# Performance work log

Hardware: AMD Instinct MI355X
Metric: run time of the kernel (lower is better)

Reference implementation:

```python
import jax, jax.numpy as jnp
import numpy as np

B = 32
M = 3
MAG_DIM = 20
STD = 0.28
INV = float(1.0 / (np.sqrt(2.0) * STD))
NORM = float(1.0 / (np.sqrt(2.0 * np.pi) * STD))


def _lrelu(x):
    return jax.nn.leaky_relu(x, 0.01)


def _conv(x, w, b):
    y = jax.lax.conv_general_dilated(x, w, (2, 2), 'VALID',
                                     dimension_numbers=('NCHW', 'OIHW', 'NCHW'))
    return _lrelu(y + b[None, :, None, None])


def _combos(x):
    # x: [N, c, d] -> [N, c, c, 2d], pairs[n, i, j] = concat(x[n, i], x[n, j])
    # (matches torch getCombinations: tensorB = expand-over-i, tensorA = expand-over-j)
    N, c, d = x.shape
    left = jnp.broadcast_to(x[:, :, None, :], (N, c, c, d))
    right = jnp.broadcast_to(x[:, None, :, :], (N, c, c, d))
    return jnp.concatenate([left, right], axis=-1)


def _forward(batch, conv_w1, conv_b1, conv_w2, conv_b2, conv_w3, conv_b3, conv_w4, conv_b4,
             post_w, post_b, g_w1, g_b1, g_w2, g_b2, g_w3, g_b3, g_w4, g_b4,
             h_w1, h_b1, h_w2, h_b2, h_w3, h_b3, f_w1, f_b1, f_w2, f_b2, ff_w, ff_b):
    bsz = batch.shape[0]
    x = batch.reshape(bsz * 16, 1, 80, 80)
    # magnitude encoding (computed under no_grad in the original)
    mag = jnp.linspace(-1.0, 1.0, MAG_DIM).astype(batch.dtype)  # [20]
    t = jnp.tanh(x * (2.0 / 255.0) - 1.0)                        # [N,1,80,80]
    enc = NORM * jnp.exp(-(((t + mag[None, :, None, None]) * INV) ** 2))  # [N,20,80,80]
    enc = jax.lax.stop_gradient(enc)
    y = _conv(enc, conv_w1, conv_b1)   # [N,32,39,39]
    y = _conv(y, conv_w2, conv_b2)     # [N,32,19,19]
    y = _conv(y, conv_w3, conv_b3)     # [N,32,9,9]
    y = _conv(y, conv_w4, conv_b4)     # [N,32,4,4]
    obj = y.reshape(bsz * 16, 512) @ post_w + post_b             # [N,247]
    panel = obj.reshape(bsz, 16, 247)
    given, options = panel[:, :8], panel[:, 8:]
    giv = jnp.broadcast_to(given[:, None], (bsz, 8, 8, 247))
    ctx = jnp.concatenate([giv, options[:, :, None, :]], axis=2)  # [B,8,9,247]
    tags = jnp.broadcast_to(jnp.eye(9, dtype=batch.dtype), (bsz * 8, 9, 9))
    objects = jnp.concatenate([ctx.reshape(bsz * 8, 9, 247), tags], axis=-1)  # [B*8,9,256]

    z = _combos(objects).reshape(-1, 512)  # [B*8*81, 512]
    z = _lrelu(z @ g_w1 + g_b1)
    z = _lrelu(z @ g_w2 + g_b2)
    z = _lrelu(z @ g_w3 + g_b3)
    z = _lrelu(z @ g_w4 + g_b4)
    sum_j = z.reshape(bsz * 8, 9, 9, 256).sum(axis=2)  # [B*8,9,256]
    for i in range(h_w1.shape[0]):
        p = _combos(sum_j).reshape(-1, 512)
        z = _lrelu(p @ h_w1[i] + h_b1[i])
        z = _lrelu(z @ h_w2[i] + h_b2[i])
        z = _lrelu(z @ h_w3[i] + h_b3[i])
        sum_j = z.reshape(bsz * 8, 9, 9, 256).sum(axis=2)
    h_sum = sum_j.sum(axis=1)                          # [B*8,256]
    z = _lrelu(h_sum @ f_w1 + f_b1)
    z = _lrelu(z @ f_w2 + f_b2)
    result = z @ ff_w + ff_b                           # [B*8,1]
    answer = result.reshape(bsz, 8)
    loss = jnp.mean(h_sum ** 2) + jnp.mean(result ** 2)
    return answer, loss


def setup_inputs():
    key = jax.random.key(0)
    ks = iter(jax.random.split(key, 40))

    def U(shape, fan_in):
        s = 1.0 / np.sqrt(fan_in)
        return jax.random.uniform(next(ks), shape, jnp.float32, -s, s)

    inp = {
        'batch': jax.random.uniform(next(ks), (B, 16, 80, 80), jnp.float32, 0.0, 255.0),
        'conv_w1': U((32, MAG_DIM, 3, 3), MAG_DIM * 9), 'conv_b1': U((32,), MAG_DIM * 9),
        'conv_w2': U((32, 32, 3, 3), 288), 'conv_b2': U((32,), 288),
        'conv_w3': U((32, 32, 3, 3), 288), 'conv_b3': U((32,), 288),
        'conv_w4': U((32, 32, 3, 3), 288), 'conv_b4': U((32,), 288),
        'post_w': U((512, 247), 512), 'post_b': U((247,), 512),
        'g_w1': U((512, 512), 512), 'g_b1': U((512,), 512),
        'g_w2': U((512, 512), 512), 'g_b2': U((512,), 512),
        'g_w3': U((512, 512), 512), 'g_b3': U((512,), 512),
        'g_w4': U((512, 256), 512), 'g_b4': U((256,), 512),
        'h_w1': U((M, 512, 256), 512), 'h_b1': U((M, 256), 512),
        'h_w2': U((M, 256, 256), 256), 'h_b2': U((M, 256), 256),
        'h_w3': U((M, 256, 256), 256), 'h_b3': U((M, 256), 256),
        'f_w1': U((256, 256), 256), 'f_b1': U((256,), 256),
        'f_w2': U((256, 256), 256), 'f_b2': U((256,), 256),
        'ff_w': U((256, 1), 256), 'ff_b': U((1,), 256),
    }
    return inp


def reference(batch, conv_w1, conv_b1, conv_w2, conv_b2, conv_w3, conv_b3, conv_w4, conv_b4,
              post_w, post_b, g_w1, g_b1, g_w2, g_b2, g_w3, g_b3, g_w4, g_b4,
              h_w1, h_b1, h_w2, h_b2, h_w3, h_b3, f_w1, f_b1, f_w2, f_b2, ff_w, ff_b):
    return _forward(batch, conv_w1, conv_b1, conv_w2, conv_b2, conv_w3, conv_b3, conv_w4, conv_b4,
                    post_w, post_b, g_w1, g_b1, g_w2, g_b2, g_w3, g_b3, g_w4, g_b4,
                    h_w1, h_b1, h_w2, h_b2, h_w3, h_b3, f_w1, f_b1, f_w2, f_b2, ff_w, ff_b)
```

## Files before the change

### kernel.cpp

```cpp
#include <hip/hip_runtime.h>
#include <hip/hip_bf16.h>
#include <math.h>

static __device__ __forceinline__ float lrelu(float v){ return v > 0.0f ? v : 0.01f*v; }

static __device__ __forceinline__ unsigned short f2bf(float f){
  unsigned int u = __float_as_uint(f);
  unsigned int r = (u + 0x7fffu + ((u >> 16) & 1u)) >> 16;
  return (unsigned short)r;
}
static __device__ __forceinline__ float bf2f(unsigned short u){
  return __uint_as_float(((unsigned int)u) << 16);
}
static __device__ __forceinline__ unsigned int pack_bf2(float lo, float hi){
  __hip_bfloat162 bb = __float22bfloat162_rn(make_float2(lo, hi));
  return *reinterpret_cast<unsigned int*>(&bb);
}
static __device__ __forceinline__ void gload16(const void* g, void* l){
  __builtin_amdgcn_global_load_lds(
    (const __attribute__((address_space(1))) void*)(const void*)g,
    (__attribute__((address_space(3))) void*)l, 16, 0, 0);
}

#define ENC_NORM 1.4247939f
#define GC_C     6.3775511f
#define GC_2CD   1.3426423f
#define GC_CD2   0.070665395f
#define GC_S1    0.86820227f

typedef __attribute__((ext_vector_type(4))) float f32x4;
typedef __attribute__((ext_vector_type(8))) short bf16x8;

__global__ __launch_bounds__(256) void k_prep(
    const float* __restrict__ g_w1, const float* __restrict__ g_w2,
    const float* __restrict__ g_w3, const float* __restrict__ g_w4,
    const float* __restrict__ h_w1, const float* __restrict__ h_w2,
    const float* __restrict__ h_w3, const float* __restrict__ post_w,
    const float* __restrict__ conv_w2, const float* __restrict__ conv_w3,
    const float* __restrict__ conv_w4, const float* __restrict__ conv_w1,
    const float* __restrict__ f_w1, const float* __restrict__ f_w2,
    unsigned short* __restrict__ WT)
{
  int e = blockIdx.x*256 + threadIdx.x;
  float v;
  if (e < 262144) {
    int nn = e >> 8, kk = e & 255;
    v = (nn < 512) ? g_w1[kk*512 + nn] : g_w1[(256+kk)*512 + (nn-512)];
  } else if (e < 524288) {
    int r = e - 262144; int nn = r >> 9, kk = r & 511;
    v = g_w2[kk*512 + nn];
  } else if (e < 786432) {
    int r = e - 524288; int nn = r >> 9, kk = r & 511;
    v = g_w3[kk*512 + nn];
  } else if (e < 917504) {
    int r = e - 786432; int nn = r >> 9, kk = r & 511;
    v = g_w4[kk*256 + nn];
  } else if (e < 1310720) {
    int r = e - 917504; int i = r >> 17; int q = r & 131071;
    int nn = q >> 8, kk = q & 255;
    v = (nn < 256) ? h_w1[i*131072 + kk*256 + nn]
                   : h_w1[i*131072 + (256+kk)*256 + (nn-256)];
  } else if (e < 1507328) {
    int r = e - 1310720; int i = r >> 16; int q = r & 65535;
    int nn = q >> 8, kk = q & 255;
    v = h_w2[i*65536 + kk*256 + nn];
  } else if (e < 1703936) {
    int r = e - 1507328; int i = r >> 16; int q = r & 65535;
    int nn = q >> 8, kk = q & 255;
    v = h_w3[i*65536 + kk*256 + nn];
  } else if (e < 1835008) {
    int r = e - 1703936; int np = r >> 9, kp = r & 511;
    int px = kp >> 5, c = kp & 31;
    v = (np < 247) ? post_w[(c*16+px)*247 + np] : 0.f;
  } else if (e < 1862656) {
    int r = e - 1835008; int which = r / 9216; int q = r % 9216;
    int tap = q >> 10, o = (q >> 5) & 31, c = q & 31;
    const float* w = which==0 ? conv_w2 : (which==1 ? conv_w3 : conv_w4);
    v = w[(o*32+c)*9 + tap];
  } else if (e < 1871872) {
    int r = e - 1862656; int tap = r >> 10, o = (r >> 5) & 31, c = r & 31;
    v = (c < 20) ? conv_w1[(o*20+c)*9 + tap] : 0.f;
  } else if (e < 1937408) {
    int r = e - 1871872; int nn = r >> 8, kk = r & 255;
    v = f_w1[kk*256 + nn];
  } else {
    int r = e - 1937408; int nn = r >> 8, kk = r & 255;
    v = f_w2[kk*256 + nn];
  }
  WT[e] = f2bf(v);
}

__global__ __launch_bounds__(256, 1) void k_conv1m(
    const float* __restrict__ batch, const unsigned short* __restrict__ wc1,
    const float* __restrict__ bias, unsigned short* __restrict__ y)
{
  __shared__ unsigned short ench[7][80][40];
  int n = blockIdx.x;
  int s0 = blockIdx.y ? 7 : 0;
  int s1 = blockIdx.y ? 13 : 7;
  int tid = threadIdx.x;
  int lane = tid & 63, wid = tid >> 6;
  int lr = lane & 15, kg = lane >> 4;

  bf16x8 bf0[9], bf1[9];
  #pragma unroll
  for (int tap = 0; tap < 9; ++tap) {
    bf0[tap] = *(const bf16x8*)&wc1[tap*1024 + lr*32 + kg*8];
    bf1[tap] = *(const bf16x8*)&wc1[tap*1024 + (16+lr)*32 + kg*8];
  }
  float b0 = bias[lr], b1 = bias[16 + lr];
  const float S2 = GC_S1 * GC_S1;

  for (int s = s0; s < s1; ++s) {
    int orow0 = s * 3;
    int irow0 = orow0 * 2;
    const float* img = batch + (size_t)n*6400 + irow0*80;
    for (int p = tid; p < 7*80; p += 256) {
      int row = p / 80, hx = p % 80;
      int col = (hx < 40) ? 2*hx : 2*(hx-40)+1;
      if (col > 78) continue;
      float x = img[row*80 + col];
      float E = __expf(x * (4.0f/255.0f) - 2.0f);
      float t = 1.0f - 2.0f*__builtin_amdgcn_rcpf(E + 1.0f);
      float z = t - 1.0f;
      float e = ENC_NORM * __expf(-GC_C*z*z);
      float rg = __expf(-GC_2CD*z - GC_CD2);
      unsigned int pk[16];
      #pragma unroll
      for (int cp = 0; cp < 10; ++cp) {
        float e1 = e * rg;
        pk[cp] = pack_bf2(e, e1);
        e  = e1 * rg * GC_S1;
        rg = rg * S2;
      }
      #pragma unroll
      for (int cp = 10; cp < 16; ++cp) pk[cp] = 0u;
      unsigned short* dst = &ench[row][hx][0];
      *(uint4*)(dst)      = *(uint4*)&pk[0];
      *(uint4*)(dst + 8)  = *(uint4*)&pk[4];
      *(uint4*)(dst + 16) = *(uint4*)&pk[8];
      *(uint4*)(dst + 24) = *(uint4*)&pk[12];
    }
    __syncthreads();

    const int totpx = 117;
    for (int t = wid; t < 8; t += 4) {
      int pa = t*16 + lr;
      int pc = (pa < totpx) ? pa : (totpx - 1);
      int oh = pc / 39, ow = pc % 39;
      f32x4 acc0 = {0.f,0.f,0.f,0.f}, acc1 = {0.f,0.f,0.f,0.f};
      #pragma unroll
      for (int kh = 0; kh < 3; ++kh) {
        int r = oh*2 + kh;
        #pragma unroll
        for (int kw = 0; kw < 3; ++kw) {
          int hidx = (kw == 1) ? (40 + ow) : (ow + (kw >> 1));
          bf16x8 a = *(const bf16x8*)&ench[r][hidx][kg*8];
          int tap = kh*3 + kw;
          acc0 = __builtin_amdgcn_mfma_f32_16x16x32_bf16(a, bf0[tap], acc0, 0, 0, 0);
          acc1 = __builtin_amdgcn_mfma_f32_16x16x32_bf16(a, bf1[tap], acc1, 0, 0, 0);
        }
      }
      #pragma unroll
      for (int rr = 0; rr < 4; ++rr) {
        int ps = t*16 + kg*4 + rr;
        if (ps < totpx) {
          int soh = orow0 + ps / 39, sow = ps % 39;
          unsigned short* op = y + (((size_t)n*39 + soh)*39 + sow)*32;
          op[lr]      = f2bf(lrelu(acc0[rr] + b0));
          op[16 + lr] = f2bf(lrelu(acc1[rr] + b1));
        }
      }
    }
    __syncthreads();
  }
}

template<int H, int W, int OH, int OW, int ROWS, int SLABS>
__global__ __launch_bounds__(256, 1) void k_cmfma(
    const unsigned short* __restrict__ in, const unsigned short* __restrict__ wc,
    const float* __restrict__ bias, unsigned short* __restrict__ out)
{
  constexpr int IR = 2*ROWS + 1;
  constexpr int EV = (W + 1) / 2;
  __shared__ unsigned short xs[IR][W][40];
  int n = blockIdx.x;
  int tid = threadIdx.x;
  int lane = tid & 63, wid = tid >> 6;
  int lr = lane & 15, kg = lane >> 4;

  bf16x8 bf0[9], bf1[9];
  #pragma unroll
  for (int tap = 0; tap < 9; ++tap) {
    bf0[tap] = *(const bf16x8*)&wc[(tap*32 + lr)*32      + kg*8];
    bf1[tap] = *(const bf16x8*)&wc[(tap*32 + 16 + lr)*32 + kg*8];
  }
  float b0 = bias[lr], b1 = bias[16 + lr];

  for (int s = 0; s < SLABS; ++s) {
    int orow0 = (blockIdx.y * SLABS + s) * ROWS;
    if (orow0 >= OH) break;
    int nrows = min(ROWS, OH - orow0);
    int irow0 = orow0 * 2;
    int ir = min(2*nrows + 1, H - irow0);

    const unsigned short* ip = in + ((size_t)n*H + irow0)*W*32;
    int npx = ir * W;
    for (int p = tid; p < npx; p += 256) {
      const uint4* src = (const uint4*)(ip + (size_t)p*32);
      uint4 v0 = src[0], v1 = src[1], v2 = src[2], v3 = src[3];
      int r = p / W, col = p % W;
      int hx = (col & 1) ? EV + (col >> 1) : (col >> 1);
      unsigned short* dst = &xs[r][hx][0];
      *(uint4*)(dst)      = v0;
      *(uint4*)(dst + 8)  = v1;
      *(uint4*)(dst + 16) = v2;
      *(uint4*)(dst + 24) = v3;
    }
    __syncthreads();

    int totpx = nrows * OW;
    int ntiles = (totpx + 15) >> 4;
    for (int t = wid; t < ntiles; t += 4) {
      int pa = t*16 + lr;
      int pc = (pa < totpx) ? pa : 0;
      int oh = pc / OW, ow = pc % OW;
      f32x4 acc0 = {0.f,0.f,0.f,0.f}, acc1 = {0.f,0.f,0.f,0.f};
      #pragma unroll
      for (int kh = 0; kh < 3; ++kh)
        #pragma unroll
        for (int kw = 0; kw < 3; ++kw) {
          int hidx = (kw == 1) ? (EV + ow) : (ow + (kw >> 1));
          bf16x8 a = *(const bf16x8*)&xs[oh*2 + kh][hidx][kg*8];
          acc0 = __builtin_amdgcn_mfma_f32_16x16x32_bf16(a, bf0[kh*3+kw], acc0, 0, 0, 0);
          acc1 = __builtin_amdgcn_mfma_f32_16x16x32_bf16(a, bf1[kh*3+kw], acc1, 0, 0, 0);
        }
      #pragma unroll
      for (int rr = 0; rr < 4; ++rr) {
        int ps = t*16 + kg*4 + rr;
        if (ps < totpx) {
          int soh = orow0 + ps / OW, sow = ps % OW;
          unsigned short* op = out + (((size_t)n*OH + soh)*OW + sow)*32;
          op[lr]      = f2bf(lrelu(acc0[rr] + b0));
          op[16 + lr] = f2bf(lrelu(acc1[rr] + b1));
        }
      }
    }
    __syncthreads();
  }
}

template<int OUT_BF16, int ACT>
__global__ __launch_bounds__(256) void k_mgemm(
    const unsigned short* __restrict__ A, const unsigned short* __restrict__ Wt,
    const float* __restrict__ bias, void* __restrict__ Cv,
    int M, int N, int K)
{
  __shared__ unsigned short As[128*64];
  __shared__ unsigned short Bs[128*64];
  int bm = blockIdx.x * 128;
  int bn = blockIdx.y * 128;
  int tid = threadIdx.x;
  int wid = tid >> 6, lane = tid & 63;
  int wr = (wid >> 1) * 64, wc = (wid & 1) * 64;
  int lr = lane & 15, kg = lane >> 4;

  int srow = lane >> 3;
  int ssw  = ((lane & 7) * 16) ^ (srow << 4);
  int rsw  = (lr & 7) << 4;

  f32x4 acc[4][4];
  #pragma unroll
  for (int i = 0; i < 4; ++i)
    #pragma unroll
    for (int j = 0; j < 4; ++j)
      acc[i][j] = (f32x4){0.f,0.f,0.f,0.f};

  for (int k0 = 0; k0 < K; k0 += 64) {
    #pragma unroll
    for (int i = 0; i < 4; ++i) {
      int rowc = wid*32 + i*8;
      int row  = rowc + srow;
      gload16((const char*)&A[(size_t)(bm + row)*K + k0] + ssw, &As[rowc*64]);
      gload16((const char*)&Wt[(size_t)(bn + row)*K + k0] + ssw, &Bs[rowc*64]);
    }
    __syncthreads();
    #pragma unroll
    for (int ks = 0; ks < 2; ++ks) {
      int roff = ((ks*64 + kg*16) ^ rsw) >> 1;
      bf16x8 a[4], b[4];
      #pragma unroll
      for (int i = 0; i < 4; ++i) {
        a[i] = *(const bf16x8*)&As[(wr + i*16 + lr)*64 + roff];
        b[i] = *(const bf16x8*)&Bs[(wc + i*16 + lr)*64 + roff];
      }
      #pragma unroll
      for (int i = 0; i < 4; ++i)
        #pragma unroll
        for (int j = 0; j < 4; ++j)
          acc[i][j] = __builtin_amdgcn_mfma_f32_16x16x32_bf16(a[i], b[j], acc[i][j], 0, 0, 0);
    }
    __syncthreads();
  }
  int r0 = (lane >> 4) * 4;
  #pragma unroll
  for (int i = 0; i < 4; ++i) {
    #pragma unroll
    for (int j = 0; j < 4; ++j) {
      int col = bn + wc + j*16 + lr;
      float bv = bias ? bias[col] : 0.f;
      #pragma unroll
      for (int rr = 0; rr < 4; ++rr) {
        int row = bm + wr + i*16 + r0 + rr;
        float v = acc[i][j][rr] + bv;
        if (ACT) v = lrelu(v);
        if (OUT_BF16) ((unsigned short*)Cv)[(size_t)row*N + col] = f2bf(v);
        else          ((float*)Cv)[(size_t)row*N + col] = v;
      }
    }
  }
}

__global__ __launch_bounds__(256) void k_pgemm(
    const unsigned short* __restrict__ UV, const unsigned short* __restrict__ Wt,
    const float* __restrict__ abias, const float* __restrict__ obias,
    unsigned short* __restrict__ C, int M, int N, int K)
{
  __shared__ unsigned short As[128*64];
  __shared__ unsigned short Bs[128*64];
  __shared__ float absm[512];
  int bm = blockIdx.x * 128;
  int bn = blockIdx.y * 128;
  int tid = threadIdx.x;
  int wid = tid >> 6, lane = tid & 63;
  int wr = (wid >> 1) * 64, wc = (wid & 1) * 64;
  int lr = lane & 15, kg = lane >> 4;
  int ld = 2*K;

  int srow = lane >> 3;
  int ssw  = ((lane & 7) * 16) ^ (srow << 4);
  int rsw  = (lr & 7) << 4;

  for (int idx = tid; idx < K; idx += 256) absm[idx] = abias[idx];

  int urow[4], vrow[4], arow[4], asw[4];
  #pragma unroll
  for (int i = 0; i < 4; ++i) {
    int ch = tid + (i << 8);
    int r = ch >> 3;
    int m = bm + r;
    int n = m / 81; int rem = m - n*81;
    int ii = rem / 9; int jj = rem - ii*9;
    urow[i] = n*9 + ii; vrow[i] = n*9 + jj;
    arow[i] = r;
    asw[i] = (((ch & 7) * 16) ^ ((r & 7) << 4)) >> 1;
  }
  __syncthreads();

  f32x4 acc[4][4];
  #pragma unroll
  for (int i = 0; i < 4; ++i)
    #pragma unroll
    for (int j = 0; j < 4; ++j)
      acc[i][j] = (f32x4){0.f,0.f,0.f,0.f};

  for (int k0 = 0; k0 < K; k0 += 64) {
    #pragma unroll
    for (int i = 0; i < 4; ++i) {
      int rowc = wid*32 + i*8;
      int row  = rowc + srow;
      gload16((const char*)&Wt[(size_t)(bn + row)*K + k0] + ssw, &Bs[rowc*64]);
    }
    #pragma unroll
    for (int i = 0; i < 4; ++i) {
      int ch = tid + (i << 8);
      int kc = (ch & 7) * 8;
      uint4 u4 = *(const uint4*)&UV[(size_t)urow[i]*ld + k0 + kc];
      uint4 v4 = *(const uint4*)&UV[(size_t)vrow[i]*ld + K + k0 + kc];
      const unsigned short* us = (const unsigned short*)&u4;
      const unsigned short* vs = (const unsigned short*)&v4;
      unsigned int pk[4];
      #pragma unroll
      for (int e2 = 0; e2 < 4; ++e2) {
        float a0 = bf2f(us[2*e2])   + bf2f(vs[2*e2])   + absm[k0 + kc + 2*e2];
        float a1 = bf2f(us[2*e2+1]) + bf2f(vs[2*e2+1]) + absm[k0 + kc + 2*e2+1];
        pk[e2] = pack_bf2(lrelu(a0), lrelu(a1));
      }
      *(uint4*)&As[arow[i]*64 + asw[i]] = *(uint4*)pk;
    }
    __syncthreads();
    #pragma unroll
    for (int ks = 0; ks < 2; ++ks) {
      int roff = ((ks*64 + kg*16) ^ rsw) >> 1;
      bf16x8 a[4], b[4];
      #pragma unroll
      for (int i = 0; i < 4; ++i) {
        a[i] = *(const bf16x8*)&As[(wr + i*16 + lr)*64 + roff];
        b[i] = *(const bf16x8*)&Bs[(wc + i*16 + lr)*64 + roff];
      }
      #pragma unroll
      for (int i = 0; i < 4; ++i)
        #pragma unroll
        for (int j = 0; j < 4; ++j)
          acc[i][j] = __builtin_amdgcn_mfma_f32_16x16x32_bf16(a[i], b[j], acc[i][j], 0, 0, 0);
    }
    __syncthreads();
  }
  int r0 = (lane >> 4) * 4;
  #pragma unroll
  for (int i = 0; i < 4; ++i) {
    #pragma unroll
    for (int j = 0; j < 4; ++j) {
      int col = bn + wc + j*16 + lr;
      float bv = obias[col];
      #pragma unroll
      for (int rr = 0; rr < 4; ++rr) {
        int row = bm + wr + i*16 + r0 + rr;
        C[(size_t)row*N + col] = f2bf(lrelu(acc[i][j][rr] + bv));
      }
    }
  }
}

__global__ void k_objects(const float* __restrict__ panel, const float* __restrict__ post_b,
                          unsigned short* __restrict__ obj)
{
  int idx = blockIdx.x*256 + threadIdx.x;
  int row = idx >> 8;
  int k = idx & 255;
  int slot = row % 9;
  int nn = row / 9;
  int b = nn >> 3, opt = nn & 7;
  float v;
  if (k < 247) {
    int src = (slot < 8) ? (b*16 + slot) : (b*16 + 8 + opt);
    v = panel[(size_t)src*256 + k] + post_b[k];
  } else {
    v = ((k - 247) == slot) ? 1.0f : 0.0f;
  }
  obj[idx] = f2bf(v);
}

__global__ void k_sumj(const unsigned short* __restrict__ Z, float* __restrict__ SJ,
                       unsigned short* __restrict__ SJb, int C)
{
  int idx = blockIdx.x*256 + threadIdx.x;
  int orow = idx / C, k = idx % C;
  int n = orow / 9, i = orow % 9;
  const unsigned short* base = Z + (size_t)(n*81 + i*9)*C + k;
  float s = 0.f;
  #pragma unroll
  for (int j = 0; j < 9; ++j) s += bf2f(base[(size_t)j*C]);
  SJ[idx] = s;
  SJb[idx] = f2bf(s);
}

__global__ void k_hsum(const float* __restrict__ SJ, float* __restrict__ HS,
                       unsigned short* __restrict__ HSb)
{
  int idx = blockIdx.x*256 + threadIdx.x;
  int n = idx >> 8, k = idx & 255;
  const float* base = SJ + (size_t)n*9*256 + k;
  float s = 0.f;
  #pragma unroll
  for (int i = 0; i < 9; ++i) s += base[i*256];
  HS[idx] = s;
  HSb[idx] = f2bf(s);
}

__global__ __launch_bounds__(256) void k_tailfin(
    const float* __restrict__ HS, const unsigned short* __restrict__ F2,
    const float* __restrict__ ffw, const float* __restrict__ ffb,
    float* __restrict__ out)
{
  __shared__ float red[256];
  __shared__ float wsm[256];
  int tid = threadIdx.x;
  wsm[tid] = ffw[tid];
  float s = 0.f;
  for (int j = 0; j < 256; ++j) { float v = HS[j*256 + tid]; s += v*v; }
  red[tid] = s; __syncthreads();
  for (int off = 128; off > 0; off >>= 1) { if (tid < off) red[tid] += red[tid + off]; __syncthreads(); }
  float hsq = red[0];
  __syncthreads();
  float r = ffb[0];
  for (int k = 0; k < 256; ++k) r += bf2f(F2[(size_t)tid*256 + k])*wsm[k];
  red[tid] = r*r; __syncthreads();
  for (int off = 128; off > 0; off >>= 1) { if (tid < off) red[tid] += red[tid + off]; __syncthreads(); }
  out[tid] = r;
  if (tid == 0) out[256] = hsq/65536.0f + red[0]/256.0f;
}

extern "C" void kernel_launch(void* const* d_in, const int* in_sizes, int n_in,
                              void* d_out, int out_size, void* d_ws, size_t ws_size,
                              hipStream_t stream)
{
  const float* batch   = (const float*)d_in[0];
  const float* conv_w1 = (const float*)d_in[1];
  const float* conv_b1 = (const float*)d_in[2];
  const float* conv_w2 = (const float*)d_in[3];
  const float* conv_b2 = (const float*)d_in[4];
  const float* conv_w3 = (const float*)d_in[5];
  const float* conv_b3 = (const float*)d_in[6];
  const float* conv_w4 = (const float*)d_in[7];
  const float* conv_b4 = (const float*)d_in[8];
  const float* post_w  = (const float*)d_in[9];
  const float* post_b  = (const float*)d_in[10];
  const float* g_w1    = (const float*)d_in[11];
  const float* g_b1    = (const float*)d_in[12];
  const float* g_w2    = (const float*)d_in[13];
  const float* g_b2    = (const float*)d_in[14];
  const float* g_w3    = (const float*)d_in[15];
  const float* g_b3    = (const float*)d_in[16];
  const float* g_w4    = (const float*)d_in[17];
  const float* g_b4    = (const float*)d_in[18];
  const float* h_w1    = (const float*)d_in[19];
  const float* h_b1    = (const float*)d_in[20];
  const float* h_w2    = (const float*)d_in[21];
  const float* h_b2    = (const float*)d_in[22];
  const float* h_w3    = (const float*)d_in[23];
  const float* h_b3    = (const float*)d_in[24];
  const float* f_w1    = (const float*)d_in[25];
  const float* f_b1    = (const float*)d_in[26];
  const float* f_w2    = (const float*)d_in[27];
  const float* f_b2    = (const float*)d_in[28];
  const float* ff_w    = (const float*)d_in[29];
  const float* ff_b    = (const float*)d_in[30];

  char* wsb = (char*)d_ws;
  const size_t off_Y1    = 0;
  const size_t off_Y2    = 52000000;
  const size_t off_Y3    = 64000000;
  const size_t off_Y4    = 67000000;
  const size_t off_PANEL = 68000000;
  const size_t off_WT    = 132000000;
  const size_t off_Pb    = 0;
  const size_t off_Qb    = 22000000;
  const size_t off_UV    = 44000000;
  const size_t off_OBJb  = 54000000;
  const size_t off_SJ    = 56000000;
  const size_t off_SJb   = 59000000;
  const size_t off_HS    = 61000000;
  const size_t off_HSb   = 61500000;
  const size_t off_F1    = 62000000;
  const size_t off_F2    = 63000000;

  unsigned short* WT = (unsigned short*)(wsb + off_WT);
  const size_t wt_g1   = 0;
  const size_t wt_g2   = 262144;
  const size_t wt_g3   = 524288;
  const size_t wt_g4   = 786432;
  const size_t wt_h1   = 917504;
  const size_t wt_h2   = 1310720;
  const size_t wt_h3   = 1507328;
  const size_t wt_post = 1703936;
  const size_t wt_cw2  = 1835008;
  const size_t wt_cw3  = 1844224;
  const size_t wt_cw4  = 1853440;
  const size_t wt_cw1  = 1862656;
  const size_t wt_f1   = 1871872;
  const size_t wt_f2   = 1937408;

  dim3 b256(256);

  k_prep<<<dim3(7824), b256, 0, stream>>>(g_w1, g_w2, g_w3, g_w4, h_w1, h_w2, h_w3,
                                          post_w, conv_w2, conv_w3, conv_w4, conv_w1,
                                          f_w1, f_w2, WT);

  unsigned short* Y1 = (unsigned short*)(wsb + off_Y1);
  unsigned short* Y2 = (unsigned short*)(wsb + off_Y2);
  unsigned short* Y3 = (unsigned short*)(wsb + off_Y3);
  unsigned short* Y4 = (unsigned short*)(wsb + off_Y4);
  float* PANEL = (float*)(wsb + off_PANEL);

  k_conv1m<<<dim3(512,2), b256, 0, stream>>>(batch, WT + wt_cw1, conv_b1, Y1);
  k_cmfma<39,39,19,19,10,2><<<dim3(512,1), b256, 0, stream>>>(Y1, WT + wt_cw2, conv_b2, Y2);
  k_cmfma<19,19, 9, 9, 9,1><<<dim3(512,1), b256, 0, stream>>>(Y2, WT + wt_cw3, conv_b3, Y3);
  k_cmfma< 9, 9, 4, 4, 4,1><<<dim3(512,1), b256, 0, stream>>>(Y3, WT + wt_cw4, conv_b4, Y4);

  k_mgemm<0,0><<<dim3(4,2), b256, 0, stream>>>(Y4, WT + wt_post, nullptr, PANEL, 512,256,512);

  unsigned short* OBJb = (unsigned short*)(wsb + off_OBJb);
  unsigned short* Pb   = (unsigned short*)(wsb + off_Pb);
  unsigned short* Qb   = (unsigned short*)(wsb + off_Qb);
  unsigned short* SJb  = (unsigned short*)(wsb + off_SJb);
  unsigned short* UVb  = (unsigned short*)(wsb + off_UV);
  float* SJ = (float*)(wsb + off_SJ);
  float* HS = (float*)(wsb + off_HS);
  unsigned short* HSb = (unsigned short*)(wsb + off_HSb);
  unsigned short* F1 = (unsigned short*)(wsb + off_F1);
  unsigned short* F2 = (unsigned short*)(wsb + off_F2);

  k_objects<<<dim3(2304), b256, 0, stream>>>(PANEL, post_b, OBJb);

  k_mgemm<1,0><<<dim3(18,8), b256, 0, stream>>>(OBJb, WT + wt_g1, nullptr, UVb, 2304,1024,256);
  k_pgemm<<<dim3(162,4), b256, 0, stream>>>(UVb, WT + wt_g2, g_b1, g_b2, Qb, 20736,512,512);
  k_mgemm<1,1><<<dim3(162,4), b256, 0, stream>>>(Qb, WT + wt_g3, g_b3, Pb, 20736,512,512);
  k_mgemm<1,1><<<dim3(162,2), b256, 0, stream>>>(Pb, WT + wt_g4, g_b4, Qb, 20736,256,512);
  k_sumj<<<dim3(2304), b256, 0, stream>>>(Qb, SJ, SJb, 256);

  for (int i = 0; i < 3; ++i) {
    k_mgemm<1,0><<<dim3(18,4), b256, 0, stream>>>(SJb, WT + wt_h1 + (size_t)i*131072, nullptr, UVb, 2304,512,256);
    k_pgemm<<<dim3(162,2), b256, 0, stream>>>(UVb, WT + wt_h2 + (size_t)i*65536, h_b1 + i*256, h_b2 + i*256, Qb, 20736,256,256);
    k_mgemm<1,1><<<dim3(162,2), b256, 0, stream>>>(Qb, WT + wt_h3 + (size_t)i*65536, h_b3 + i*256, Pb, 20736,256,256);
    k_sumj<<<dim3(2304), b256, 0, stream>>>(Pb, SJ, SJb, 256);
  }

  k_hsum<<<dim3(256), b256, 0, stream>>>(SJ, HS, HSb);
  k_mgemm<1,1><<<dim3(2,2), b256, 0, stream>>>(HSb, WT + wt_f1, f_b1, F1, 256,256,256);
  k_mgemm<1,1><<<dim3(2,2), b256, 0, stream>>>(F1,  WT + wt_f2, f_b2, F2, 256,256,256);
  k_tailfin<<<dim3(1), b256, 0, stream>>>(HS, F2, ff_w, ff_b, (float*)d_out);
}
```

Baseline: 349.0 us.

## Split conv1 by column halves, halve conv2 row slabs, vectorize reduction kernels

conv1 now splits each image's work across the two y-blocks by output column half instead of by row slab. Each block keeps a smaller 7x41 LDS tile, and each of the four waves handles one 16-pixel tile per slab. conv2 uses 5-row slabs on a doubled grid to add parallelism. The sumj and hsum reductions switch to 8-wide bf16 and float4 vector loads and stores with fewer threads, cutting per-element memory transactions. In exchange, conv1 recomputes the overlapping encoded column at the split, and each wave now runs 13 slab iterations, so the loop is longer per block.

```diff
diff --git a/kernel.cpp b/kernel.cpp
--- a/kernel.cpp
+++ b/kernel.cpp
@@ -94,10 +94,12 @@
     const float* __restrict__ batch, const unsigned short* __restrict__ wc1,
     const float* __restrict__ bias, unsigned short* __restrict__ y)
 {
-  __shared__ unsigned short ench[7][80][40];
+  __shared__ unsigned short ench[7][41][40];
   int n = blockIdx.x;
-  int s0 = blockIdx.y ? 7 : 0;
-  int s1 = blockIdx.y ? 13 : 7;
+  int h = blockIdx.y;
+  int c0 = h * 40;
+  int OWH = h ? 19 : 20;
+  int owbase = h * 20;
   int tid = threadIdx.x;
   int lane = tid & 63, wid = tid >> 6;
   int lr = lane & 15, kg = lane >> 4;
@@ -111,15 +113,16 @@
   float b0 = bias[lr], b1 = bias[16 + lr];
   const float S2 = GC_S1 * GC_S1;
 
-  for (int s = s0; s < s1; ++s) {
+  for (int s = 0; s < 13; ++s) {
     int orow0 = s * 3;
     int irow0 = orow0 * 2;
     const float* img = batch + (size_t)n*6400 + irow0*80;
-    for (int p = tid; p < 7*80; p += 256) {
-      int row = p / 80, hx = p % 80;
-      int col = (hx < 40) ? 2*hx : 2*(hx-40)+1;
-      if (col > 78) continue;
-      float x = img[row*80 + col];
+    for (int p = tid; p < 7*41; p += 256) {
+      int row = p / 41, hx = p % 41;
+      int lc = (hx < 21) ? 2*hx : 2*(hx-21)+1;
+      int c = c0 + lc;
+      if (c > 78) continue;
+      float x = img[row*80 + c];
       float E = __expf(x * (4.0f/255.0f) - 2.0f);
       float t = 1.0f - 2.0f*__builtin_amdgcn_rcpf(E + 1.0f);
       float z = t - 1.0f;
@@ -143,18 +146,19 @@
     }
     __syncthreads();
 
-    const int totpx = 117;
-    for (int t = wid; t < 8; t += 4) {
+    int totpx = 3 * OWH;
+    {
+      int t = wid;
       int pa = t*16 + lr;
       int pc = (pa < totpx) ? pa : (totpx - 1);
-      int oh = pc / 39, ow = pc % 39;
+      int ohl = pc / OWH, lw = pc % OWH;
       f32x4 acc0 = {0.f,0.f,0.f,0.f}, acc1 = {0.f,0.f,0.f,0.f};
       #pragma unroll
       for (int kh = 0; kh < 3; ++kh) {
-        int r = oh*2 + kh;
+        int r = ohl*2 + kh;
         #pragma unroll
         for (int kw = 0; kw < 3; ++kw) {
-          int hidx = (kw == 1) ? (40 + ow) : (ow + (kw >> 1));
+          int hidx = (kw == 1) ? (21 + lw) : (lw + (kw >> 1));
           bf16x8 a = *(const bf16x8*)&ench[r][hidx][kg*8];
           int tap = kh*3 + kw;
           acc0 = __builtin_amdgcn_mfma_f32_16x16x32_bf16(a, bf0[tap], acc0, 0, 0, 0);
@@ -165,7 +169,7 @@
       for (int rr = 0; rr < 4; ++rr) {
         int ps = t*16 + kg*4 + rr;
         if (ps < totpx) {
-          int soh = orow0 + ps / 39, sow = ps % 39;
+          int soh = orow0 + ps / OWH, sow = owbase + ps % OWH;
           unsigned short* op = y + (((size_t)n*39 + soh)*39 + sow)*32;
           op[lr]      = f2bf(lrelu(acc0[rr] + b0));
           op[16 + lr] = f2bf(lrelu(acc1[rr] + b1));
@@ -445,27 +449,45 @@
                        unsigned short* __restrict__ SJb, int C)
 {
   int idx = blockIdx.x*256 + threadIdx.x;
-  int orow = idx / C, k = idx % C;
+  int vpr = C >> 3;
+  int orow = idx / vpr, kv = (idx - orow*vpr) << 3;
   int n = orow / 9, i = orow % 9;
-  const unsigned short* base = Z + (size_t)(n*81 + i*9)*C + k;
-  float s = 0.f;
-  #pragma unroll
-  for (int j = 0; j < 9; ++j) s += bf2f(base[(size_t)j*C]);
-  SJ[idx] = s;
-  SJb[idx] = f2bf(s);
+  const unsigned short* base = Z + (size_t)(n*81 + i*9)*C + kv;
+  float s[8];
+  #pragma unroll
+  for (int e = 0; e < 8; ++e) s[e] = 0.f;
+  #pragma unroll
+  for (int j = 0; j < 9; ++j) {
+    bf16x8 v = *(const bf16x8*)(base + (size_t)j*C);
+    #pragma unroll
+    for (int e = 0; e < 8; ++e) s[e] += bf2f(((const unsigned short*)&v)[e]);
+  }
+  float* so = SJ + (size_t)orow*C + kv;
+  #pragma unroll
+  for (int e = 0; e < 8; ++e) so[e] = s[e];
+  unsigned int pk[4];
+  #pragma unroll
+  for (int e2 = 0; e2 < 4; ++e2) pk[e2] = pack_bf2(s[2*e2], s[2*e2+1]);
+  *(uint4*)(SJb + (size_t)orow*C + kv) = *(uint4*)pk;
 }
 
 __global__ void k_hsum(const float* __restrict__ SJ, float* __restrict__ HS,
                        unsigned short* __restrict__ HSb)
 {
   int idx = blockIdx.x*256 + threadIdx.x;
-  int n = idx >> 8, k = idx & 255;
-  const float* base = SJ + (size_t)n*9*256 + k;
-  float s = 0.f;
-  #pragma unroll
-  for (int i = 0; i < 9; ++i) s += base[i*256];
-  HS[idx] = s;
-  HSb[idx] = f2bf(s);
+  int n = idx >> 6, kc = (idx & 63) << 2;
+  const float* base = SJ + (size_t)n*9*256 + kc;
+  float4 s = {0.f,0.f,0.f,0.f};
+  #pragma unroll
+  for (int i = 0; i < 9; ++i) {
+    float4 v = *(const float4*)(base + (size_t)i*256);
+    s.x += v.x; s.y += v.y; s.z += v.z; s.w += v.w;
+  }
+  *(float4*)(HS + (size_t)n*256 + kc) = s;
+  unsigned int pk[2];
+  pk[0] = pack_bf2(s.x, s.y);
+  pk[1] = pack_bf2(s.z, s.w);
+  *(uint2*)(HSb + (size_t)n*256 + kc) = *(uint2*)pk;
 }
 
 __global__ __launch_bounds__(256) void k_tailfin(
@@ -574,7 +596,7 @@
   float* PANEL = (float*)(wsb + off_PANEL);
 
   k_conv1m<<<dim3(512,2), b256, 0, stream>>>(batch, WT + wt_cw1, conv_b1, Y1);
-  k_cmfma<39,39,19,19,10,2><<<dim3(512,1), b256, 0, stream>>>(Y1, WT + wt_cw2, conv_b2, Y2);
+  k_cmfma<39,39,19,19, 5,2><<<dim3(512,2), b256, 0, stream>>>(Y1, WT + wt_cw2, conv_b2, Y2);
   k_cmfma<19,19, 9, 9, 9,1><<<dim3(512,1), b256, 0, stream>>>(Y2, WT + wt_cw3, conv_b3, Y3);
   k_cmfma< 9, 9, 4, 4, 4,1><<<dim3(512,1), b256, 0, stream>>>(Y3, WT + wt_cw4, conv_b4, Y4);
 
@@ -597,16 +619,16 @@
   k_pgemm<<<dim3(162,4), b256, 0, stream>>>(UVb, WT + wt_g2, g_b1, g_b2, Qb, 20736,512,512);
   k_mgemm<1,1><<<dim3(162,4), b256, 0, stream>>>(Qb, WT + wt_g3, g_b3, Pb, 20736,512,512);
   k_mgemm<1,1><<<dim3(162,2), b256, 0, stream>>>(Pb, WT + wt_g4, g_b4, Qb, 20736,256,512);
-  k_sumj<<<dim3(2304), b256, 0, stream>>>(Qb, SJ, SJb, 256);
+  k_sumj<<<dim3(288), b256, 0, stream>>>(Qb, SJ, SJb, 256);
 
   for (int i = 0; i < 3; ++i) {
     k_mgemm<1,0><<<dim3(18,4), b256, 0, stream>>>(SJb, WT + wt_h1 + (size_t)i*131072, nullptr, UVb, 2304,512,256);
     k_pgemm<<<dim3(162,2), b256, 0, stream>>>(UVb, WT + wt_h2 + (size_t)i*65536, h_b1 + i*256, h_b2 + i*256, Qb, 20736,256,256);
     k_mgemm<1,1><<<dim3(162,2), b256, 0, stream>>>(Qb, WT + wt_h3 + (size_t)i*65536, h_b3 + i*256, Pb, 20736,256,256);
-    k_sumj<<<dim3(2304), b256, 0, stream>>>(Pb, SJ, SJb, 256);
-  }
-
-  k_hsum<<<dim3(256), b256, 0, stream>>>(SJ, HS, HSb);
+    k_sumj<<<dim3(288), b256, 0, stream>>>(Pb, SJ, SJb, 256);
+  }
+
+  k_hsum<<<dim3(64), b256, 0, stream>>>(SJ, HS, HSb);
   k_mgemm<1,1><<<dim3(2,2), b256, 0, stream>>>(HSb, WT + wt_f1, f_b1, F1, 256,256,256);
   k_mgemm<1,1><<<dim3(2,2), b256, 0, stream>>>(F1,  WT + wt_f2, f_b2, F2, 256,256,256);
   k_tailfin<<<dim3(1), b256, 0, stream>>>(HS, F2, ff_w, ff_b, (float*)d_out);
```

Measured after the change: 340.4 us. -2.5%, faster.
